# Kernel optimization log

Measured on AMD Instinct MI355X. Metric: run time of the kernel, lower is better.

The kernel has to match this reference:

```python
import jax, jax.numpy as jnp
import numpy as np

EPS = 1e-12  # matches torch.nn.functional.normalize eps


def _normalize(x):
    n = jnp.sqrt(jnp.sum(x * x, axis=-1, keepdims=True))
    return x / jnp.maximum(n, EPS)


def setup_inputs() -> dict:
    key = jax.random.key(0)
    k1, k2, k3 = jax.random.split(key, 3)
    B, C, D = 1024, 32768, 512
    embeddings = jax.random.normal(k1, (B, D), dtype=jnp.float32)
    proxies = jax.random.normal(k2, (C, D), dtype=jnp.float32) / 8.0
    labels = jax.random.randint(k3, (B,), 0, C, dtype=jnp.int64)
    return {"embeddings": embeddings, "proxies": proxies, "labels": labels}


def reference(embeddings, proxies, labels):
    # batch: [B, D], P: [C, D], both scaled to norm 3
    batch = 3.0 * _normalize(embeddings)
    P = 3.0 * _normalize(proxies)

    # Squared euclidean distances to ALL proxies via the expansion
    # ||b - p||^2 = ||b||^2 + ||p||^2 - 2 b.p  -> [B, C]
    b_sq = jnp.sum(batch * batch, axis=-1, keepdims=True)      # [B, 1]
    p_sq = jnp.sum(P * P, axis=-1)                             # [C]
    dist = b_sq + p_sq[None, :] - 2.0 * (batch @ P.T)          # [B, C]

    B = batch.shape[0]
    rows = jnp.arange(B)
    pos_dist = dist[rows, labels]                              # [B]

    # logsumexp over negatives: mask out the positive class per row
    neg_scores = jnp.where(
        jnp.arange(dist.shape[1])[None, :] == labels[:, None],
        -jnp.inf,
        -dist,
    )
    neg_lse = jax.nn.logsumexp(neg_scores, axis=1)             # [B]

    return jnp.mean(pos_dist + neg_lse)
```

## Files before the change

kernel.cpp:

```cpp
#include <hip/hip_runtime.h>
#include <stdint.h>

#define D_DIM 512
#define B_ROWS 1024
#define C_ROWS 32768
#define NBLK (C_ROWS / 128)

typedef __attribute__((ext_vector_type(8))) short short8;
typedef __attribute__((ext_vector_type(4))) float floatx4;

#define GLOBAL_AS __attribute__((address_space(1)))
#define LDS_AS __attribute__((address_space(3)))

__device__ inline unsigned short f2bf(float f) {
    unsigned u = __float_as_uint(f);
    u += 0x7fffu + ((u >> 16) & 1u);
    return (unsigned short)(u >> 16);
}

__device__ inline void async_copy16(const unsigned short* g, unsigned short* l) {
    __builtin_amdgcn_global_load_lds((const GLOBAL_AS void*)g, (LDS_AS void*)l, 16, 0, 0);
}

__global__ void norm_rows_kernel(const float* __restrict__ src,
                                 unsigned short* __restrict__ dst, int nrows) {
    const int wid = threadIdx.x >> 6;
    const int lane = threadIdx.x & 63;
    const int row = blockIdx.x * 4 + wid;
    if (row >= nrows) return;

    const float4* p = (const float4*)(src + (size_t)row * D_DIM + lane * 8);
    float4 v0 = p[0];
    float4 v1 = p[1];
    float ss = v0.x * v0.x + v0.y * v0.y + v0.z * v0.z + v0.w * v0.w +
               v1.x * v1.x + v1.y * v1.y + v1.z * v1.z + v1.w * v1.w;
#pragma unroll
    for (int off = 1; off < 64; off <<= 1) ss += __shfl_xor(ss, off);
    const float s = 3.0f * rsqrtf(ss);

    unsigned short h[8];
    h[0] = f2bf(v0.x * s); h[1] = f2bf(v0.y * s);
    h[2] = f2bf(v0.z * s); h[3] = f2bf(v0.w * s);
    h[4] = f2bf(v1.x * s); h[5] = f2bf(v1.y * s);
    h[6] = f2bf(v1.z * s); h[7] = f2bf(v1.w * s);
    uint4 packed;
    packed.x = (unsigned)h[0] | ((unsigned)h[1] << 16);
    packed.y = (unsigned)h[2] | ((unsigned)h[3] << 16);
    packed.z = (unsigned)h[4] | ((unsigned)h[5] << 16);
    packed.w = (unsigned)h[6] | ((unsigned)h[7] << 16);
    *(uint4*)(dst + (size_t)row * D_DIM + lane * 8) = packed;
}

__global__ void __launch_bounds__(256)
gemm_lse_kernel(const unsigned short* __restrict__ A,
                const unsigned short* __restrict__ Bm,
                float* __restrict__ part) {
    __shared__ unsigned short sA[2][128 * 32];
    __shared__ unsigned short sB[2][128 * 32];
    __shared__ float red[128];

    const int tid = threadIdx.x;
    const int wid = tid >> 6;
    const int lane = tid & 63;
    const int m0 = blockIdx.y * 128;
    const int n0 = blockIdx.x * 128;

    if (tid < 128) red[tid] = 0.f;

    const int srow = wid * 16 + (lane >> 2);
    const int skoff = (lane & 3) * 8;
    const unsigned short* gA = A + (size_t)(m0 + srow) * D_DIM + skoff;
    const unsigned short* gB = Bm + (size_t)(n0 + srow) * D_DIM + skoff;
    const int loff = srow * 32 + skoff;

    const int wm = (wid >> 1) * 64;
    const int wn = (wid & 1) * 64;
    const int fr = lane & 15;
    const int fk = (lane >> 4) * 8;
    const int quad = lane >> 4;

    floatx4 acc[4][4];
    const floatx4 zero = {0.f, 0.f, 0.f, 0.f};
#pragma unroll
    for (int i = 0; i < 4; ++i)
#pragma unroll
        for (int j = 0; j < 4; ++j) acc[i][j] = zero;

    for (int kk = 0; kk < D_DIM; kk += 64) {
        async_copy16(gA + kk,                  &sA[0][loff]);
        async_copy16(gA + kk + 64 * D_DIM,     &sA[0][loff + 64 * 32]);
        async_copy16(gA + kk + 32,             &sA[1][loff]);
        async_copy16(gA + kk + 32 + 64 * D_DIM, &sA[1][loff + 64 * 32]);
        async_copy16(gB + kk,                  &sB[0][loff]);
        async_copy16(gB + kk + 64 * D_DIM,     &sB[0][loff + 64 * 32]);
        async_copy16(gB + kk + 32,             &sB[1][loff]);
        async_copy16(gB + kk + 32 + 64 * D_DIM, &sB[1][loff + 64 * 32]);
        __syncthreads();

#pragma unroll
        for (int c = 0; c < 2; ++c) {
            short8 af[4], bfv[4];
#pragma unroll
            for (int t = 0; t < 4; ++t) {
                af[t]  = *(const short8*)&sA[c][(wm + t * 16 + fr) * 32 + fk];
                bfv[t] = *(const short8*)&sB[c][(wn + t * 16 + fr) * 32 + fk];
            }
#pragma unroll
            for (int ti = 0; ti < 4; ++ti)
#pragma unroll
                for (int tj = 0; tj < 4; ++tj)
                    acc[ti][tj] = __builtin_amdgcn_mfma_f32_16x16x32_bf16(
                        af[ti], bfv[tj], acc[ti][tj], 0, 0, 0);
        }
        __syncthreads();
    }

#pragma unroll
    for (int ti = 0; ti < 4; ++ti) {
        float rs[4] = {0.f, 0.f, 0.f, 0.f};
#pragma unroll
        for (int tj = 0; tj < 4; ++tj)
#pragma unroll
            for (int r = 0; r < 4; ++r)
                rs[r] += __expf(2.0f * acc[ti][tj][r]);
#pragma unroll
        for (int r = 0; r < 4; ++r) {
            rs[r] += __shfl_xor(rs[r], 1);
            rs[r] += __shfl_xor(rs[r], 2);
            rs[r] += __shfl_xor(rs[r], 4);
            rs[r] += __shfl_xor(rs[r], 8);
        }
        if (fr == 0) {
#pragma unroll
            for (int r = 0; r < 4; ++r)
                atomicAdd(&red[wm + ti * 16 + quad * 4 + r], rs[r]);
        }
    }
    __syncthreads();
    if (tid < 128) part[(size_t)(m0 + tid) * NBLK + blockIdx.x] = red[tid];
}

__global__ void rowloss_kernel(const float* __restrict__ part,
                               const unsigned short* __restrict__ A,
                               const unsigned short* __restrict__ Bm,
                               const int* __restrict__ labels,
                               float* __restrict__ rowloss) {
    const int wid = threadIdx.x >> 6;
    const int lane = threadIdx.x & 63;
    const int b = blockIdx.x * 4 + wid;
    if (b >= B_ROWS) return;

    float4 pv = *(const float4*)&part[(size_t)b * NBLK + lane * 4];
    float s = pv.x + pv.y + pv.z + pv.w;

    const int l = labels[b];
    uint4 ua = *(const uint4*)(A + (size_t)b * D_DIM + lane * 8);
    uint4 ub = *(const uint4*)(Bm + (size_t)l * D_DIM + lane * 8);
    const unsigned* au = (const unsigned*)&ua;
    const unsigned* bu = (const unsigned*)&ub;
    float d = 0.f;
#pragma unroll
    for (int j = 0; j < 4; ++j) {
        float a0 = __uint_as_float(au[j] << 16);
        float a1 = __uint_as_float(au[j] & 0xffff0000u);
        float b0 = __uint_as_float(bu[j] << 16);
        float b1 = __uint_as_float(bu[j] & 0xffff0000u);
        d += a0 * b0 + a1 * b1;
    }
#pragma unroll
    for (int off = 1; off < 64; off <<= 1) {
        s += __shfl_xor(s, off);
        d += __shfl_xor(d, off);
    }
    if (lane == 0) {
        float p2 = 2.0f * d;
        rowloss[b] = logf(s - __expf(p2)) - p2;
    }
}

__global__ void finalize_kernel(const float* __restrict__ rowloss,
                                float* __restrict__ out) {
    __shared__ float red[4];
    const int tid = threadIdx.x;
    float local = 0.f;
    for (int b = tid; b < B_ROWS; b += 256) local += rowloss[b];
#pragma unroll
    for (int off = 1; off < 64; off <<= 1) local += __shfl_xor(local, off);
    const int wid = tid >> 6;
    const int lane = tid & 63;
    if (lane == 0) red[wid] = local;
    __syncthreads();
    if (tid == 0) out[0] = (red[0] + red[1] + red[2] + red[3]) / (float)B_ROWS;
}

extern "C" void kernel_launch(void* const* d_in, const int* in_sizes, int n_in,
                              void* d_out, int out_size, void* d_ws, size_t ws_size,
                              hipStream_t stream) {
    const float* emb = (const float*)d_in[0];
    const float* prox = (const float*)d_in[1];
    const int* labels = (const int*)d_in[2];
    float* out = (float*)d_out;

    char* ws = (char*)d_ws;
    unsigned short* Pbf = (unsigned short*)ws;
    unsigned short* Abf = (unsigned short*)(ws + (size_t)C_ROWS * D_DIM * 2);
    float* part = (float*)(ws + (size_t)C_ROWS * D_DIM * 2 + (size_t)B_ROWS * D_DIM * 2);
    float* rowloss = part + (size_t)B_ROWS * NBLK;

    norm_rows_kernel<<<C_ROWS / 4, 256, 0, stream>>>(prox, Pbf, C_ROWS);
    norm_rows_kernel<<<B_ROWS / 4, 256, 0, stream>>>(emb, Abf, B_ROWS);
    gemm_lse_kernel<<<dim3(NBLK, B_ROWS / 128), 256, 0, stream>>>(Abf, Pbf, part);
    rowloss_kernel<<<B_ROWS / 4, 256, 0, stream>>>(part, Abf, Pbf, labels, rowloss);
    finalize_kernel<<<1, 256, 0, stream>>>(rowloss, out);
}
```

Baseline: 155.6 us.

## Swizzle LDS tiles, reorder GEMM grid, and merge normalization launches

Applies an XOR-style rotation of the 16-byte k-chunks in the LDS tiles so the MFMA fragment reads spread across banks instead of conflicting. Swaps the grid axes so consecutive blocks share the same proxy tile across the eight batch tiles, improving L2 reuse of the large proxy matrix. Fuses the two normalization launches into one. The swizzle must match between the async global-to-LDS writes and the fragment reads, so it adds index arithmetic and correctness risk.

```diff
diff --git a/kernel.cpp b/kernel.cpp
--- a/kernel.cpp
+++ b/kernel.cpp
@@ -22,12 +22,21 @@
     __builtin_amdgcn_global_load_lds((const GLOBAL_AS void*)g, (LDS_AS void*)l, 16, 0, 0);
 }
 
-__global__ void norm_rows_kernel(const float* __restrict__ src,
-                                 unsigned short* __restrict__ dst, int nrows) {
+__global__ void norm_rows_kernel(const float* __restrict__ prox,
+                                 const float* __restrict__ emb,
+                                 unsigned short* __restrict__ Pbf,
+                                 unsigned short* __restrict__ Abf) {
     const int wid = threadIdx.x >> 6;
     const int lane = threadIdx.x & 63;
-    const int row = blockIdx.x * 4 + wid;
-    if (row >= nrows) return;
+    int row = blockIdx.x * 4 + wid;
+    const float* src;
+    unsigned short* dst;
+    if (row < C_ROWS) {
+        src = prox; dst = Pbf;
+    } else {
+        row -= C_ROWS;
+        src = emb; dst = Abf;
+    }
 
     const float4* p = (const float4*)(src + (size_t)row * D_DIM + lane * 8);
     float4 v0 = p[0];
@@ -62,22 +71,23 @@
     const int tid = threadIdx.x;
     const int wid = tid >> 6;
     const int lane = tid & 63;
-    const int m0 = blockIdx.y * 128;
-    const int n0 = blockIdx.x * 128;
+    const int m0 = blockIdx.x * 128;
+    const int n0 = blockIdx.y * 128;
 
     if (tid < 128) red[tid] = 0.f;
 
     const int srow = wid * 16 + (lane >> 2);
-    const int skoff = (lane & 3) * 8;
-    const unsigned short* gA = A + (size_t)(m0 + srow) * D_DIM + skoff;
-    const unsigned short* gB = Bm + (size_t)(n0 + srow) * D_DIM + skoff;
-    const int loff = srow * 32 + skoff;
+    const int sg = lane & 3;
+    const int gl = (sg - ((lane >> 3) & 3)) & 3;
+    const unsigned short* gA = A + (size_t)(m0 + srow) * D_DIM + gl * 8;
+    const unsigned short* gB = Bm + (size_t)(n0 + srow) * D_DIM + gl * 8;
+    const int loff = srow * 32 + sg * 8;
 
     const int wm = (wid >> 1) * 64;
     const int wn = (wid & 1) * 64;
     const int fr = lane & 15;
-    const int fk = (lane >> 4) * 8;
     const int quad = lane >> 4;
+    const int swz = (((quad + ((fr >> 1) & 3)) & 3) * 8);
 
     floatx4 acc[4][4];
     const floatx4 zero = {0.f, 0.f, 0.f, 0.f};
@@ -87,13 +97,13 @@
         for (int j = 0; j < 4; ++j) acc[i][j] = zero;
 
     for (int kk = 0; kk < D_DIM; kk += 64) {
-        async_copy16(gA + kk,                  &sA[0][loff]);
-        async_copy16(gA + kk + 64 * D_DIM,     &sA[0][loff + 64 * 32]);
-        async_copy16(gA + kk + 32,             &sA[1][loff]);
+        async_copy16(gA + kk,                   &sA[0][loff]);
+        async_copy16(gA + kk + 64 * D_DIM,      &sA[0][loff + 64 * 32]);
+        async_copy16(gA + kk + 32,              &sA[1][loff]);
         async_copy16(gA + kk + 32 + 64 * D_DIM, &sA[1][loff + 64 * 32]);
-        async_copy16(gB + kk,                  &sB[0][loff]);
-        async_copy16(gB + kk + 64 * D_DIM,     &sB[0][loff + 64 * 32]);
-        async_copy16(gB + kk + 32,             &sB[1][loff]);
+        async_copy16(gB + kk,                   &sB[0][loff]);
+        async_copy16(gB + kk + 64 * D_DIM,      &sB[0][loff + 64 * 32]);
+        async_copy16(gB + kk + 32,              &sB[1][loff]);
         async_copy16(gB + kk + 32 + 64 * D_DIM, &sB[1][loff + 64 * 32]);
         __syncthreads();
 
@@ -102,8 +112,8 @@
             short8 af[4], bfv[4];
 #pragma unroll
             for (int t = 0; t < 4; ++t) {
-                af[t]  = *(const short8*)&sA[c][(wm + t * 16 + fr) * 32 + fk];
-                bfv[t] = *(const short8*)&sB[c][(wn + t * 16 + fr) * 32 + fk];
+                af[t]  = *(const short8*)&sA[c][(wm + t * 16 + fr) * 32 + swz];
+                bfv[t] = *(const short8*)&sB[c][(wn + t * 16 + fr) * 32 + swz];
             }
 #pragma unroll
             for (int ti = 0; ti < 4; ++ti)
@@ -137,7 +147,7 @@
         }
     }
     __syncthreads();
-    if (tid < 128) part[(size_t)(m0 + tid) * NBLK + blockIdx.x] = red[tid];
+    if (tid < 128) part[(size_t)(m0 + tid) * NBLK + blockIdx.y] = red[tid];
 }
 
 __global__ void rowloss_kernel(const float* __restrict__ part,
@@ -207,9 +217,8 @@
     float* part = (float*)(ws + (size_t)C_ROWS * D_DIM * 2 + (size_t)B_ROWS * D_DIM * 2);
     float* rowloss = part + (size_t)B_ROWS * NBLK;
 
-    norm_rows_kernel<<<C_ROWS / 4, 256, 0, stream>>>(prox, Pbf, C_ROWS);
-    norm_rows_kernel<<<B_ROWS / 4, 256, 0, stream>>>(emb, Abf, B_ROWS);
-    gemm_lse_kernel<<<dim3(NBLK, B_ROWS / 128), 256, 0, stream>>>(Abf, Pbf, part);
+    norm_rows_kernel<<<(C_ROWS + B_ROWS) / 4, 256, 0, stream>>>(prox, emb, Pbf, Abf);
+    gemm_lse_kernel<<<dim3(B_ROWS / 128, NBLK), 256, 0, stream>>>(Abf, Pbf, part);
     rowloss_kernel<<<B_ROWS / 4, 256, 0, stream>>>(part, Abf, Pbf, labels, rowloss);
     finalize_kernel<<<1, 256, 0, stream>>>(rowloss, out);
 }
```

After: 153.4 us. Within noise of the previous version (-1.5%).
